# Performance work log

Hardware: AMD Instinct MI355X
Metric: run time of the kernel (lower is better)

## Reference

```python
import jax, jax.numpy as jnp
import numpy as np

NE, EW, TOP_K, T_D, MAXNNZ = 32, 2944, 4, 8, 256
ALPHA, LIMIT, ORIG = 1.702, 7.0, 2880
HID = 2048


def setup_inputs() -> dict:
    key = jax.random.key(0)
    ks = jax.random.split(key, 7)
    dt = jnp.float16
    hid = jax.random.normal(ks[0], (1, 1024, HID), dtype=dt)
    # rand_init() sets all params to torch.rand(...)/5 -> Uniform[0, 0.2)
    gate_w = (jax.random.uniform(ks[1], (NE, HID), dtype=dt) * 0.2).astype(dt)
    u = (jax.random.uniform(ks[2], (NE * EW, HID), dtype=dt) * 0.2).astype(dt)
    g = (jax.random.uniform(ks[3], (NE * EW, HID), dtype=dt) * 0.2).astype(dt)
    d = (jax.random.uniform(ks[4], (HID, NE * EW), dtype=dt) * 0.2).astype(dt)
    ub = (jax.random.uniform(ks[5], (NE * EW,), dtype=dt) * 0.2).astype(dt)
    gb = (jax.random.uniform(ks[6], (NE * EW,), dtype=dt) * 0.2).astype(dt)
    return {"hid": hid, "gate_w": gate_w, "u": u, "g": g, "d": d, "ub": ub, "gb": gb}


def _act(up, gate):
    # clamped GLU: gate clamped above, up clamped both sides; glu = g*sigmoid(alpha*g); (up+1)*glu
    gate = jnp.minimum(gate, LIMIT)
    up = jnp.clip(up, -LIMIT, LIMIT)
    glu = gate * jax.nn.sigmoid(gate * ALPHA)
    act = (up + 1.0) * glu
    return act.at[..., ORIG:].set(0)  # padded inter dims (2880..2944) zeroed


def _forward(hid, gate_w, u, g, d, ub, gb):
    B, S, H = hid.shape
    x = hid.reshape(-1, H)           # [bs, H]
    bs = x.shape[0]

    # --- routing: softmax -> top-k -> renormalize -> scatter to sparse weights ---
    logits = (x @ gate_w.T).astype(jnp.float32)          # [bs, NE]
    probs = jax.nn.softmax(logits, axis=1)
    vals, idx = jax.lax.top_k(probs, TOP_K)
    vals = vals / vals.sum(axis=1, keepdims=True)
    sparse_rw = jnp.zeros_like(probs).at[jnp.arange(bs)[:, None], idx].set(vals)
    rw = sparse_rw.astype(x.dtype)                        # [bs, NE]

    # --- expert selection: t_d dense experts + t_d sparse experts by load ---
    routing_n = jnp.count_nonzero(rw, axis=0)
    mask_c = jax.lax.top_k(routing_n, 2 * T_D)[1]         # [2*T_D]
    cd, cs = mask_c[:T_D], mask_c[T_D:]
    # top-MAXNNZ tokens per sparse expert
    mask_r = jax.lax.top_k(sparse_rw[:, cs].T, MAXNNZ)[1].T  # [MAXNNZ, T_D]

    U = u.reshape(NE, EW, H)
    G = g.reshape(NE, EW, H)
    UB = ub.reshape(NE, EW)
    GB = gb.reshape(NE, EW)
    D = d.reshape(H, NE, EW)

    # --- dense experts: every token runs through the t_d hottest experts ---
    up_d = jnp.einsum('nh,teh->nte', x, U[cd]) + UB[cd]   # [bs, T_D, EW]
    gt_d = jnp.einsum('nh,teh->nte', x, G[cd]) + GB[cd]
    act_d = _act(up_d, gt_d) * rw[:, cd][..., None]       # routing weight combine
    out = jnp.einsum('nte,hte->nh', act_d, D[:, cd])      # [bs, H]

    # --- sparse experts: gather top-MAXNNZ tokens, MLP, scatter-add back ---
    xs = x[mask_r]                                        # [M, T_D, H]
    up_s = jnp.einsum('mth,teh->mte', xs, U[cs]) + UB[cs]
    gt_s = jnp.einsum('mth,teh->mte', xs, G[cs]) + GB[cs]
    w_s = rw[mask_r, cs[None, :]]                         # [M, T_D]
    act_s = _act(up_s, gt_s) * w_s[..., None]
    contrib = jnp.einsum('mte,hte->mth', act_s, D[:, cs])  # [M, T_D, H]
    out = out.at[mask_r.reshape(-1)].add(contrib.reshape(-1, H))

    return out.reshape(B, S, H)


def reference(hid, gate_w, u, g, d, ub, gb):
    return _forward(hid, gate_w, u, g, d, ub, gb)
```

## Files before the change

### kernel.cpp

```cpp
#include <hip/hip_runtime.h>

#define HID 2048
#define NE_ 32
#define EW_ 2944
#define ORIG_ 2880
#define TOPK_ 4
#define MAXNNZ_ 256
#define BS_ 1024
#define NEWTOT (NE_*EW_)

typedef unsigned short u16;
typedef _Float16 h8  __attribute__((ext_vector_type(8)));
typedef float  f32x4 __attribute__((ext_vector_type(4)));
typedef float  fv4   __attribute__((ext_vector_type(4)));

__device__ __forceinline__ u16 f2h_bits(float f){
  union{ _Float16 h; u16 u; } c; c.h = (_Float16)f; return c.u;
}
__device__ __forceinline__ float f16q(float f){ return (float)(_Float16)f; }

__device__ __forceinline__ h8 cvt8(fv4 a, fv4 b){
  h8 r;
  r[0]=(_Float16)a[0]; r[1]=(_Float16)a[1]; r[2]=(_Float16)a[2]; r[3]=(_Float16)a[3];
  r[4]=(_Float16)b[0]; r[5]=(_Float16)b[1]; r[6]=(_Float16)b[2]; r[7]=(_Float16)b[3];
  return r;
}
__device__ __forceinline__ int ldsx(int row, int chunk){
  return row*32 + ((chunk ^ ((row>>1)&3))*8);
}

__device__ __forceinline__ void barrier_lgkm(){
  asm volatile("s_waitcnt lgkmcnt(0)" ::: "memory");
  __builtin_amdgcn_s_barrier();
  __builtin_amdgcn_sched_barrier(0);
}

__device__ __forceinline__ int rank_kth(const int* counts, int kth){
  int cnt[NE_]; bool used[NE_];
  for (int e=0;e<NE_;e++){ cnt[e]=counts[e]; used[e]=false; }
  int bi=0;
  for (int k=0;k<=kth;k++){
    int best=-1; bi=0;
    for (int e=0;e<NE_;e++) if(!used[e] && cnt[e]>best){best=cnt[e];bi=e;}
    used[bi]=true;
  }
  return bi;
}

__global__ __launch_bounds__(256) void k_gate(const float* __restrict__ x,
                                              const float* __restrict__ gw,
                                              float* __restrict__ rw,
                                              float* __restrict__ rwf,
                                              int* __restrict__ counts,
                                              u16* __restrict__ xh)
{
  __shared__ float slog[4][NE_];
  const int tid = threadIdx.x, wid = tid>>6, lane = tid&63;
  const int n = blockIdx.x*4 + wid;
  const float* xr = x + (size_t)n*HID + lane*32;
  float xf[32];
  #pragma unroll
  for (int i=0;i<8;i++){
    fv4 v = *(const fv4*)(xr + i*4);
    #pragma unroll
    for (int j=0;j<4;j++) xf[i*4+j] = v[j];
  }
  #pragma unroll
  for (int c=0;c<4;c++){
    h8 hv;
    #pragma unroll
    for (int j=0;j<8;j++) hv[j] = (_Float16)xf[c*8+j];
    *(h8*)(xh + (size_t)n*HID + lane*32 + c*8) = hv;
  }
  for (int e=0;e<NE_;e++){
    const float* gr = gw + (size_t)e*HID + lane*32;
    float p = 0.f;
    #pragma unroll
    for (int i=0;i<8;i++){
      fv4 v = *(const fv4*)(gr + i*4);
      #pragma unroll
      for (int j=0;j<4;j++) p += xf[i*4+j]*v[j];
    }
    #pragma unroll
    for (int s=32;s>0;s>>=1) p += __shfl_xor(p, s);
    if (lane==0) slog[wid][e] = f16q(p);
  }
  if (lane==0){
    float mx=-1e30f;
    for (int e=0;e<NE_;e++) mx = fmaxf(mx, slog[wid][e]);
    float pr[NE_]; float sum=0.f;
    for (int e=0;e<NE_;e++){ float v=__expf(slog[wid][e]-mx); pr[e]=v; sum+=v; }
    for (int e=0;e<NE_;e++) pr[e] = pr[e]/sum;
    int   idx[TOPK_]; float val[TOPK_]; bool used[NE_];
    for (int e=0;e<NE_;e++) used[e]=false;
    float vs=0.f;
    for (int k=0;k<TOPK_;k++){
      float best=-1.f; int bi=0;
      for (int e=0;e<NE_;e++) if(!used[e] && pr[e]>best){best=pr[e];bi=e;}
      used[bi]=true; idx[k]=bi; val[k]=best; vs+=best;
    }
    float* rwr  = rw  + (size_t)n*NE_;
    float* rwfr = rwf + (size_t)n*NE_;
    for (int k=0;k<TOPK_;k++){
      float vraw = val[k]/vs;
      float q = f16q(vraw);
      rwr[idx[k]]  = q;
      rwfr[idx[k]] = vraw;
      if (q!=0.f) atomicAdd(counts+idx[k], 1);
    }
  }
}

__global__ __launch_bounds__(256) void k_lists(const float* __restrict__ rw,
                                               const float* __restrict__ rwf,
                                               const int* __restrict__ counts,
                                               int* __restrict__ cdcs,
                                               int* __restrict__ tok_all,
                                               int* __restrict__ cnt_all,
                                               int* __restrict__ inv,
                                               int* __restrict__ invcnt)
{
  const int z = blockIdx.x, q = blockIdx.y;
  const int tid = threadIdx.x;
  const int e = rank_kth(counts, z);
  if (q==0 && tid==0) cdcs[z] = e;
  const int i = q*256 + tid;
  bool take;
  if (z<8){
    take = (rw[(size_t)i*NE_+e] != 0.f);
  } else {
    const float vi = rwf[(size_t)i*NE_+e];
    int r=0;
    for (int m=0;m<BS_;m++){
      float vm = rwf[(size_t)m*NE_+e];
      r += (vm>vi) || (vm==vi && m<i);
    }
    take = (r<MAXNNZ_) && (rw[(size_t)i*NE_+e]!=0.f);
  }
  if (take){
    int slot = atomicAdd(&cnt_all[z], 1);
    tok_all[z*BS_+slot] = i;
    int c = atomicAdd(&invcnt[i], 1);
    inv[i*4+c] = (z<<16) | slot;
  }
}

#define FSTEP(P, KT)                                                        \
{                                                                           \
  u16* A = ldsA[(P)&1]; u16* B = ldsB[(P)&1];                               \
  _Pragma("unroll")                                                         \
  for (int r=0;r<4;r++) *(h8*)&A[ldsx(ar + r*64, ach)] = Aset[(P)&1][r];    \
  *(h8*)&B[ldsx(br, ach)] = cvt8(Bsa[(P)], Bsb[(P)]);                       \
  if ((KT)+2 < NKF){                                                        \
    const int k2 = ((KT)+2)*32;                                             \
    _Pragma("unroll")                                                       \
    for (int r=0;r<4;r++) Aset[(P)&1][r] = *(const h8*)(ap[r]+k2);          \
  }                                                                         \
  if ((KT)+4 < NKF){                                                        \
    const int k4 = ((KT)+4)*32;                                             \
    Bsa[(P)] = *(const fv4*)(bp+k4); Bsb[(P)] = *(const fv4*)(bp+k4+4);     \
  }                                                                         \
  barrier_lgkm();                                                           \
  h8 af[4], fu[2], fg[2];                                                   \
  _Pragma("unroll")                                                         \
  for (int m=0;m<4;m++) af[m] = *(const h8*)&A[ldsx(w*64+m*16+lr, kq)];     \
  _Pragma("unroll")                                                         \
  for (int n2=0;n2<2;n2++){                                                 \
    fu[n2] = *(const h8*)&B[ldsx(   n2*16+lr, kq)];                         \
    fg[n2] = *(const h8*)&B[ldsx(32+n2*16+lr, kq)];                         \
  }                                                                         \
  _Pragma("unroll")                                                         \
  for (int m=0;m<4;m++)                                                     \
    _Pragma("unroll")                                                       \
    for (int n2=0;n2<2;n2++){                                               \
      au[m][n2]=__builtin_amdgcn_mfma_f32_16x16x32_f16(af[m],fu[n2],au[m][n2],0,0,0); \
      ag[m][n2]=__builtin_amdgcn_mfma_f32_16x16x32_f16(af[m],fg[n2],ag[m][n2],0,0,0); \
    }                                                                       \
}

__global__ __launch_bounds__(256, 2) void k_fused(const u16* __restrict__ xh,
                                               const float* __restrict__ uw,
                                               const float* __restrict__ gww,
                                               const float* __restrict__ ub,
                                               const float* __restrict__ gb,
                                               const float* __restrict__ rw,
                                               const int* __restrict__ cdcs,
                                               const int* __restrict__ tok_all,
                                               const int* __restrict__ cnt_all,
                                               u16* __restrict__ act)
{
  const int z=blockIdx.z, bx=blockIdx.x, by=blockIdx.y;
  const int cnt = cnt_all[z];
  if (by*256 >= cnt) return;
  const int e = cdcs[z];
  __shared__ __align__(16) u16 ldsA[2][256*32];
  __shared__ __align__(16) u16 ldsB[2][64*32];
  const int tid=threadIdx.x, lane=tid&63, w=tid>>6;
  const int lr = lane&15, kq = lane>>4;
  const int ar = tid>>2, ach = tid&3;
  const u16* ap[4];
  #pragma unroll
  for (int r=0;r<4;r++){
    const int tok = tok_all[z*BS_ + by*256 + ar + r*64];
    ap[r] = xh + (size_t)tok*HID + ach*8;
  }
  const int br = ar;
  const float* bp = (br<32 ? uw  + ((size_t)e*EW_ + bx*32 + br)*HID
                           : gww + ((size_t)e*EW_ + bx*32 + (br-32))*HID) + ach*8;

  f32x4 au[4][2], ag[4][2];
  #pragma unroll
  for (int i=0;i<4;i++)
    #pragma unroll
    for (int j=0;j<2;j++)
      #pragma unroll
      for (int q=0;q<4;q++){ au[i][j][q]=0.f; ag[i][j][q]=0.f; }

  h8 Aset[2][4]; fv4 Bsa[4], Bsb[4];
  #pragma unroll
  for (int r=0;r<4;r++){
    Aset[0][r] = *(const h8*)ap[r];
    Aset[1][r] = *(const h8*)(ap[r]+32);
  }
  #pragma unroll
  for (int p=0;p<4;p++){
    Bsa[p] = *(const fv4*)(bp+p*32); Bsb[p] = *(const fv4*)(bp+p*32+4);
  }

  const int NKF = HID/32;
  for (int kt=0; kt<NKF; kt+=4){
    FSTEP(0, kt)
    FSTEP(1, kt+1)
    FSTEP(2, kt+2)
    FSTEP(3, kt+3)
  }

  #pragma unroll
  for (int n2=0;n2<2;n2++){
    const int col = bx*32 + n2*16 + lr;
    const float ubv = ub[(size_t)e*EW_ + col];
    const float gbv = gb[(size_t)e*EW_ + col];
    #pragma unroll
    for (int m=0;m<4;m++){
      #pragma unroll
      for (int j=0;j<4;j++){
        const int s = by*256 + w*64 + m*16 + kq*4 + j;
        if (s < cnt){
          float upv = f16q(au[m][n2][j] + ubv);
          float gtv = f16q(ag[m][n2][j] + gbv);
          float wv = rw[(size_t)tok_all[z*BS_+s]*NE_ + e];
          float gc = fminf(gtv, 7.0f);
          float uc = fminf(fmaxf(upv,-7.0f),7.0f);
          float glu = gc * (1.f/(1.f+__expf(-gc*1.702f)));
          act[((size_t)z*BS_+s)*ORIG_ + col] = f2h_bits((uc+1.f)*glu*wv);
        }
      }
    }
  }
}

#define DSTEP(P, KT)                                                        \
{                                                                           \
  u16* A = ldsA[(P)&1]; u16* B = ldsB[(P)&1];                               \
  _Pragma("unroll")                                                         \
  for (int r=0;r<4;r++) *(h8*)&A[ldsx(ar + r*64, ach)] = Aset[(P)&1][r];    \
  *(h8*)&B[ldsx(br, ach)] = cvt8(Bsa[(P)], Bsb[(P)]);                       \
  if ((KT)+2 < NKD){                                                        \
    const int k2 = ((KT)+2)*32;                                             \
    _Pragma("unroll")                                                       \
    for (int r=0;r<4;r++) Aset[(P)&1][r] = *(const h8*)(ap[r]+k2);          \
  }                                                                         \
  if ((KT)+4 < NKD){                                                        \
    const int k4 = ((KT)+4)*32;                                             \
    Bsa[(P)] = *(const fv4*)(bp+k4); Bsb[(P)] = *(const fv4*)(bp+k4+4);     \
  }                                                                         \
  barrier_lgkm();                                                           \
  h8 af[4], bfr[4];                                                         \
  _Pragma("unroll")                                                         \
  for (int m=0;m<4;m++)    af[m]  = *(const h8*)&A[ldsx(w*64+m*16+lr, kq)]; \
  _Pragma("unroll")                                                         \
  for (int n2=0;n2<4;n2++) bfr[n2] = *(const h8*)&B[ldsx(n2*16+lr, kq)];    \
  _Pragma("unroll")                                                         \
  for (int m=0;m<4;m++)                                                     \
    _Pragma("unroll")                                                       \
    for (int n2=0;n2<4;n2++)                                                \
      acc[m][n2]=__builtin_amdgcn_mfma_f32_16x16x32_f16(af[m],bfr[n2],acc[m][n2],0,0,0); \
}

__global__ __launch_bounds__(256, 2) void k_down(const u16* __restrict__ act,
                                              const float* __restrict__ dw,
                                              const int* __restrict__ cdcs,
                                              const int* __restrict__ cnt_all,
                                              u16* __restrict__ contrib)
{
  const int zz=blockIdx.z, bx=blockIdx.x, by=blockIdx.y;
  const int z = zz>>1, kh = zz&1;
  const int cnt = cnt_all[z];
  if (by*256 >= cnt) return;
  const int e = cdcs[z];
  __shared__ __align__(16) u16 ldsA[2][256*32];
  __shared__ __align__(16) u16 ldsB[2][64*32];
  const int tid=threadIdx.x, lane=tid&63, w=tid>>6;
  const int lr = lane&15, kq = lane>>4;
  const int ar = tid>>2, ach = tid&3;
  const int kbase = kh*1440;

  const u16* ap[4];
  #pragma unroll
  for (int r=0;r<4;r++)
    ap[r] = act + ((size_t)z*BS_ + by*256 + ar + r*64)*ORIG_ + kbase + ach*8;
  const int br = ar;
  const float* bp = dw + (size_t)(bx*64 + br)*NEWTOT + (size_t)e*EW_ + kbase + ach*8;

  f32x4 acc[4][4];
  #pragma unroll
  for (int i=0;i<4;i++)
    #pragma unroll
    for (int j=0;j<4;j++)
      #pragma unroll
      for (int q=0;q<4;q++) acc[i][j][q]=0.f;

  h8 Aset[2][4]; fv4 Bsa[4], Bsb[4];
  #pragma unroll
  for (int r=0;r<4;r++){
    Aset[0][r] = *(const h8*)ap[r];
    Aset[1][r] = *(const h8*)(ap[r]+32);
  }
  #pragma unroll
  for (int p=0;p<4;p++){
    Bsa[p] = *(const fv4*)(bp+p*32); Bsb[p] = *(const fv4*)(bp+p*32+4);
  }

  const int NKD = 1440/32;
  for (int kt=0; kt<44; kt+=4){
    DSTEP(0, kt)
    DSTEP(1, kt+1)
    DSTEP(2, kt+2)
    DSTEP(3, kt+3)
  }
  DSTEP(0, 44)

  #pragma unroll
  for (int m=0;m<4;m++){
    #pragma unroll
    for (int j=0;j<4;j++){
      const int slot = by*256 + w*64 + m*16 + kq*4 + j;
      if (slot < cnt){
        #pragma unroll
        for (int n2=0;n2<4;n2++){
          const int col = bx*64 + n2*16 + lr;
          contrib[((size_t)zz*BS_ + slot)*HID + col] = f2h_bits(acc[m][n2][j]);
        }
      }
    }
  }
}

__global__ __launch_bounds__(256) void k_combine(const u16* __restrict__ contrib,
                                                 const int* __restrict__ inv,
                                                 const int* __restrict__ invcnt,
                                                 float* __restrict__ out)
{
  const int gid = blockIdx.x*256 + threadIdx.x;
  const int base = gid*8;
  const int n = base >> 11;
  const int h = base & 2047;
  float acc[8];
  #pragma unroll
  for (int q=0;q<8;q++) acc[q]=0.f;
  const int c = invcnt[n];
  for (int j=0;j<c;j++){
    const int code = inv[n*4+j];
    const int z = code>>16;
    const int slot = code & 0xFFFF;
    const u16* p = contrib + ((size_t)(z*2)*BS_ + slot)*HID + h;
    h8 v0 = *(const h8*)p;
    h8 v1 = *(const h8*)(p + (size_t)BS_*HID);
    #pragma unroll
    for (int q=0;q<8;q++) acc[q] += (float)v0[q] + (float)v1[q];
  }
  fv4 o0, o1;
  #pragma unroll
  for (int q=0;q<4;q++){ o0[q]=acc[q]; o1[q]=acc[4+q]; }
  *(fv4*)(out + base) = o0;
  *(fv4*)(out + base + 4) = o1;
}

extern "C" void kernel_launch(void* const* d_in, const int* in_sizes, int n_in,
                              void* d_out, int out_size, void* d_ws, size_t ws_size,
                              hipStream_t stream)
{
  const float* x  = (const float*)d_in[0];
  const float* gw = (const float*)d_in[1];
  const float* u  = (const float*)d_in[2];
  const float* g  = (const float*)d_in[3];
  const float* dw = (const float*)d_in[4];
  const float* ub = (const float*)d_in[5];
  const float* gb = (const float*)d_in[6];

  char* ws = (char*)d_ws;
  size_t off = 0;
  auto alloc = [&](size_t bytes)->void*{ void* p = ws + off; off += (bytes + 255) & ~(size_t)255; return p; };
  float* rw     = (float*)alloc((size_t)BS_*NE_*4);
  float* rwf    = (float*)alloc((size_t)BS_*NE_*4);
  int*   counts = (int*)  alloc(NE_*4);
  int*   invcnt = (int*)  alloc(BS_*4);
  int*   cnt_all= (int*)  alloc(16*4);
  int*   tok_all= (int*)  alloc((size_t)16*BS_*4);
  size_t zero_span = off;
  int*   cdcs   = (int*)  alloc(16*4);
  int*   inv    = (int*)  alloc((size_t)BS_*4*4);
  u16*   xh     = (u16*)  alloc((size_t)BS_*HID*2);
  u16*   act    = (u16*)  alloc((size_t)16*BS_*ORIG_*2);
  u16*   contrib= (u16*)  alloc((size_t)32*BS_*HID*2);
  if (off > ws_size) return;

  hipMemsetAsync(ws, 0, zero_span, stream);

  k_gate <<<BS_/4, 256, 0, stream>>>(x, gw, rw, rwf, counts, xh);
  k_lists<<<dim3(16,4), 256, 0, stream>>>(rw, rwf, counts, cdcs, tok_all,
                                          cnt_all, inv, invcnt);

  k_fused<<<dim3(ORIG_/32, 4, 16), 256, 0, stream>>>(xh, u, g, ub, gb, rw,
                                                     cdcs, tok_all, cnt_all, act);
  k_down <<<dim3(HID/64, 4, 32), 256, 0, stream>>>(act, dw, cdcs, cnt_all, contrib);
  k_combine<<<BS_*HID/(256*8), 256, 0, stream>>>(contrib, inv, invcnt, (float*)d_out);
}
```

Measured before the change: 541.3 us.

## Remap grids for XCD-local expert reuse and drop split-K in down projection

Both MoE GEMM kernels now use a flat 1D grid whose block index is decoded so that each XCD (bid&7) handles a contiguous range of (expert, column-tile) pairs, with the four token tiles of a pair on the same XCD. The aim is to share expert weight tiles in that XCD's L2. The down-projection no longer splits K into two halves: each block runs the full 2880-wide reduction, which halves the contrib buffer and the combine kernel's reads. The cost is half as many down blocks, each with twice the serial work, so there is less parallelism to hide latency.

```diff
diff --git a/kernel.cpp b/kernel.cpp
--- a/kernel.cpp
+++ b/kernel.cpp
@@ -189,7 +189,11 @@
                                                const int* __restrict__ cnt_all,
                                                u16* __restrict__ act)
 {
-  const int z=blockIdx.z, bx=blockIdx.x, by=blockIdx.y;
+  const int bid = blockIdx.x;
+  const int xcd = bid & 7, t = bid >> 3;
+  const int by = t & 3, pr = t >> 2;
+  const int pair = xcd*180 + pr;
+  const int z = pair / 90, bx = pair % 90;
   const int cnt = cnt_all[z];
   if (by*256 >= cnt) return;
   const int e = cdcs[z];
@@ -293,8 +297,11 @@
                                               const int* __restrict__ cnt_all,
                                               u16* __restrict__ contrib)
 {
-  const int zz=blockIdx.z, bx=blockIdx.x, by=blockIdx.y;
-  const int z = zz>>1, kh = zz&1;
+  const int bid = blockIdx.x;
+  const int xcd = bid & 7, t = bid >> 3;
+  const int by = t & 3, pr = t >> 2;
+  const int pair = xcd*64 + pr;
+  const int z = pair / 32, bx = pair % 32;
   const int cnt = cnt_all[z];
   if (by*256 >= cnt) return;
   const int e = cdcs[z];
@@ -303,14 +310,13 @@
   const int tid=threadIdx.x, lane=tid&63, w=tid>>6;
   const int lr = lane&15, kq = lane>>4;
   const int ar = tid>>2, ach = tid&3;
-  const int kbase = kh*1440;
 
   const u16* ap[4];
   #pragma unroll
   for (int r=0;r<4;r++)
-    ap[r] = act + ((size_t)z*BS_ + by*256 + ar + r*64)*ORIG_ + kbase + ach*8;
+    ap[r] = act + ((size_t)z*BS_ + by*256 + ar + r*64)*ORIG_ + ach*8;
   const int br = ar;
-  const float* bp = dw + (size_t)(bx*64 + br)*NEWTOT + (size_t)e*EW_ + kbase + ach*8;
+  const float* bp = dw + (size_t)(bx*64 + br)*NEWTOT + (size_t)e*EW_ + ach*8;
 
   f32x4 acc[4][4];
   #pragma unroll
@@ -331,14 +337,15 @@
     Bsa[p] = *(const fv4*)(bp+p*32); Bsb[p] = *(const fv4*)(bp+p*32+4);
   }
 
-  const int NKD = 1440/32;
-  for (int kt=0; kt<44; kt+=4){
+  const int NKD = ORIG_/32;
+  for (int kt=0; kt<88; kt+=4){
     DSTEP(0, kt)
     DSTEP(1, kt+1)
     DSTEP(2, kt+2)
     DSTEP(3, kt+3)
   }
-  DSTEP(0, 44)
+  DSTEP(0, 88)
+  DSTEP(1, 89)
 
   #pragma unroll
   for (int m=0;m<4;m++){
@@ -349,7 +356,7 @@
         #pragma unroll
         for (int n2=0;n2<4;n2++){
           const int col = bx*64 + n2*16 + lr;
-          contrib[((size_t)zz*BS_ + slot)*HID + col] = f2h_bits(acc[m][n2][j]);
+          contrib[((size_t)z*BS_ + slot)*HID + col] = f2h_bits(acc[m][n2][j]);
         }
       }
     }
@@ -373,11 +380,10 @@
     const int code = inv[n*4+j];
     const int z = code>>16;
     const int slot = code & 0xFFFF;
-    const u16* p = contrib + ((size_t)(z*2)*BS_ + slot)*HID + h;
+    const u16* p = contrib + ((size_t)z*BS_ + slot)*HID + h;
     h8 v0 = *(const h8*)p;
-    h8 v1 = *(const h8*)(p + (size_t)BS_*HID);
-    #pragma unroll
-    for (int q=0;q<8;q++) acc[q] += (float)v0[q] + (float)v1[q];
+    #pragma unroll
+    for (int q=0;q<8;q++) acc[q] += (float)v0[q];
   }
   fv4 o0, o1;
   #pragma unroll
@@ -412,7 +418,7 @@
   int*   inv    = (int*)  alloc((size_t)BS_*4*4);
   u16*   xh     = (u16*)  alloc((size_t)BS_*HID*2);
   u16*   act    = (u16*)  alloc((size_t)16*BS_*ORIG_*2);
-  u16*   contrib= (u16*)  alloc((size_t)32*BS_*HID*2);
+  u16*   contrib= (u16*)  alloc((size_t)16*BS_*HID*2);
   if (off > ws_size) return;
 
   hipMemsetAsync(ws, 0, zero_span, stream);
@@ -421,8 +427,8 @@
   k_lists<<<dim3(16,4), 256, 0, stream>>>(rw, rwf, counts, cdcs, tok_all,
                                           cnt_all, inv, invcnt);
 
-  k_fused<<<dim3(ORIG_/32, 4, 16), 256, 0, stream>>>(xh, u, g, ub, gb, rw,
-                                                     cdcs, tok_all, cnt_all, act);
-  k_down <<<dim3(HID/64, 4, 32), 256, 0, stream>>>(act, dw, cdcs, cnt_all, contrib);
+  k_fused<<<5760, 256, 0, stream>>>(xh, u, g, ub, gb, rw,
+                                    cdcs, tok_all, cnt_all, act);
+  k_down <<<2048, 256, 0, stream>>>(act, dw, cdcs, cnt_all, contrib);
   k_combine<<<BS_*HID/(256*8), 256, 0, stream>>>(contrib, inv, invcnt, (float*)d_out);
 }
```

New measurement: 1.370 ms. +153.1%, slower.
